# Optimization experiments

Measured on AMD Instinct MI355X. Metric: run time of the kernel, lower is better.

Reference implementation:

```python
import jax, jax.numpy as jnp
import numpy as np


def _lstm_layer(x, W_ih, W_hh, b_ih, b_hh):
    """Single unidirectional LSTM layer, PyTorch gate order (i, f, g, o).

    x: [B, T, I]; W_ih: [4H, I]; W_hh: [4H, H]; b_ih, b_hh: [4H].
    Returns all hidden states: [B, T, H].
    """
    B, T, _ = x.shape
    H = W_hh.shape[1]
    # Precompute input projections for all timesteps (one big GEMM): [B, T, 4H]
    x_proj = jnp.einsum('bti,gi->btg', x, W_ih) + b_ih + b_hh

    def step(carry, xt):
        h, c = carry
        gates = xt + h @ W_hh.T  # [B, 4H]
        i, f, g, o = jnp.split(gates, 4, axis=-1)
        c = jax.nn.sigmoid(f) * c + jax.nn.sigmoid(i) * jnp.tanh(g)
        h = jax.nn.sigmoid(o) * jnp.tanh(c)
        return (h, c), h

    init = (jnp.zeros((B, H), x.dtype), jnp.zeros((B, H), x.dtype))
    _, hs = jax.lax.scan(step, init, x_proj.transpose(1, 0, 2))  # hs: [T, B, H]
    return hs.transpose(1, 0, 2)


def setup_inputs() -> dict:
    key = jax.random.key(0)
    ks = jax.random.split(key, 16)
    B, C, T, F = 32, 4, 1024, 128
    I = C * F  # 512 = input_size
    H = 512   # hidden_size
    O = 80    # output_size (mel bins)
    s = 1.0 / np.sqrt(H)  # PyTorch LSTM/Linear init range
    inp = {'X_batch': jax.random.normal(ks[0], (B, C, T, F), jnp.float32)}
    in_sizes = [I, H, H]
    for l in range(3):
        k = 1 + 4 * l
        inp[f'W_ih_{l}'] = jax.random.uniform(ks[k + 0], (4 * H, in_sizes[l]), jnp.float32, -s, s)
        inp[f'W_hh_{l}'] = jax.random.uniform(ks[k + 1], (4 * H, H), jnp.float32, -s, s)
        inp[f'b_ih_{l}'] = jax.random.uniform(ks[k + 2], (4 * H,), jnp.float32, -s, s)
        inp[f'b_hh_{l}'] = jax.random.uniform(ks[k + 3], (4 * H,), jnp.float32, -s, s)
    inp['W_out'] = jax.random.uniform(ks[13], (O, H), jnp.float32, -s, s)
    inp['b_out'] = jax.random.uniform(ks[14], (O,), jnp.float32, -s, s)
    return inp


def reference(X_batch, W_ih_0, W_hh_0, b_ih_0, b_hh_0,
              W_ih_1, W_hh_1, b_ih_1, b_hh_1,
              W_ih_2, W_hh_2, b_ih_2, b_hh_2,
              W_out, b_out):
    B, C, T, F = X_batch.shape
    # [B, C, T, F] -> [B, T, C, F] -> [B, T, C*F], matching the torch permute+reshape
    x = X_batch.transpose(0, 2, 1, 3).reshape(B, T, C * F)
    layers = [(W_ih_0, W_hh_0, b_ih_0, b_hh_0),
              (W_ih_1, W_hh_1, b_ih_1, b_hh_1),
              (W_ih_2, W_hh_2, b_ih_2, b_hh_2)]
    for W_ih, W_hh, b_ih, b_hh in layers:
        x = _lstm_layer(x, W_ih, W_hh, b_ih, b_hh)
    last = x[:, -1, :]  # return_sequence=False: last timestep only, [B, H]
    # dropout is identity in eval mode
    return last @ W_out.T + b_out  # [B, O]
```

## Files before the change

### kernel.cpp

```cpp
#include <hip/hip_runtime.h>
#include <cstdint>


typedef unsigned short u16;
typedef _Float16 f16;
typedef f16 f16x8 __attribute__((ext_vector_type(8)));
typedef unsigned short ushort8 __attribute__((ext_vector_type(8)));
typedef float f32x4 __attribute__((ext_vector_type(4)));

#define NB 32
#define NT 1024
#define NH 512
#define N4H 2048
#define RR 16
#define MROWS (NB * NT)
#define HBUFB 8192

__device__ __forceinline__ float sigm(float x) { return 1.f / (1.f + __expf(-x)); }
__device__ __forceinline__ float tanh_s(float x) {
  float a = fabsf(x);
  float e = __expf(-2.f * a);
  float t = (1.f - e) / (1.f + e);
  return copysignf(t, x);
}

__device__ __forceinline__ void ld16_sc(const u16* p, uint4& d) {
  asm volatile("global_load_dwordx4 %0, %1, off sc0 sc1" : "=v"(d) : "v"(p));
}
__device__ __forceinline__ int ldf(const int* p) {
  int r;
  asm volatile("global_load_dword %0, %1, off sc0 sc1\n\ts_waitcnt vmcnt(0)"
               : "=v"(r) : "v"(p) : "memory");
  return r;
}
__device__ __forceinline__ void st16b_sc(u16* p, unsigned v) {
  asm volatile("global_store_short %0, %1, off sc0 sc1" :: "v"(p), "v"(v) : "memory");
}
__device__ __forceinline__ void st32b_sc(int* p, int v) {
  asm volatile("global_store_dword %0, %1, off sc0 sc1" :: "v"(p), "v"(v) : "memory");
}

__global__ void k_gather_x(const float* __restrict__ X, u16* __restrict__ xs) {
  int64_t i = (int64_t)blockIdx.x * 256 + threadIdx.x;
  int k = (int)(i & 511);
  int t = (int)((i >> 9) & 1023);
  int b = (int)(i >> 19);
  int c = k >> 7, f = k & 127;
  float v = X[(((int64_t)(b * 4 + c) * 1024 + t) << 7) + f];
  f16 hv = (f16)v;
  xs[((int64_t)b * 1024 + t) * 512 + k] = *(u16*)&hv;
}

__global__ void k_split_w(const float* __restrict__ W, u16* __restrict__ Wp) {
  int i = blockIdx.x * 256 + threadIdx.x;
  f16 hv = (f16)W[i];
  Wp[i] = *(u16*)&hv;
}

__global__ void k_bias(const float* __restrict__ bi, const float* __restrict__ bh,
                       float* __restrict__ bo) {
  int i = blockIdx.x * 256 + threadIdx.x;
  if (i < N4H) bo[i] = bi[i] + bh[i];
}

__launch_bounds__(256, 1)
__global__ void k_lstm3(const float* __restrict__ Whh0, const float* __restrict__ Whh1,
                        const float* __restrict__ Whh2,
                        const u16* __restrict__ Wp0, const u16* __restrict__ Wp1,
                        const u16* __restrict__ Wp2,
                        const float* __restrict__ bias0, const float* __restrict__ bias1,
                        const float* __restrict__ bias2,
                        const u16* __restrict__ xs, u16* __restrict__ hring,
                        u16* __restrict__ hfinal, int* __restrict__ flags) {
  __shared__ u16 wlds[32768];
  __shared__ u16 hbuf[16384];
  const int tid = threadIdx.x;
  const int lane = tid & 63;
  const int w = tid >> 6;
  const int wg = blockIdx.x;
  const int l = wg >> 6;
  const int wgl = wg & 63;
  const int bg = wgl >> 5;
  const int ugg = wgl & 31;
  const int q = lane >> 4;
  const int cb = lane & 15;
  const int tr = lane & 15;

  const float* Whh = (l == 0) ? Whh0 : (l == 1) ? Whh1 : Whh2;
  const u16* Wp = (l == 0) ? Wp0 : (l == 1) ? Wp1 : Wp2;
  const float* bs = (l == 0) ? bias0 : (l == 1) ? bias1 : bias2;

  const int64_t grow = (int64_t)(tr & 3) * 512 + ugg * 16 + w * 4 + (tr >> 2);

  f16x8 whh[16];
  {
    const float* wsrc = Whh + grow * 512 + q * 8;
#pragma unroll
    for (int kk = 0; kk < 16; ++kk) {
      float4 a = *(const float4*)(wsrc + kk * 32);
      float4 b = *(const float4*)(wsrc + kk * 32 + 4);
      f16x8 hv;
      hv[0] = (f16)a.x; hv[1] = (f16)a.y; hv[2] = (f16)a.z; hv[3] = (f16)a.w;
      hv[4] = (f16)b.x; hv[5] = (f16)b.y; hv[6] = (f16)b.z; hv[7] = (f16)b.w;
      whh[kk] = hv;
    }
  }

  {
#pragma unroll
    for (int i = 0; i < 16; ++i) {
      int c = tid + i * 256;
      int r = c >> 6;
      int kc = (c & 63) * 8;
      int tr2 = r & 15;
      int64_t gr = (int64_t)(tr2 & 3) * 512 + ugg * 16 + (r >> 4) * 4 + (tr2 >> 2);
      ushort8 v = *(const ushort8*)(Wp + gr * 512 + kc);
      *(ushort8*)&wlds[r * 512 + (kc ^ ((tr2 & 7) << 3))] = v;
    }
  }
  __syncthreads();

  const int bat = bg * 16 + cb;
  const int ucol = ugg * 16 + w * 4 + q;
  const float b0 = bs[ucol], b1 = bs[512 + ucol], b2 = bs[1024 + ucol],
              b3 = bs[1536 + ucol];
  float cst = 0.f;

  int* fl_own = flags + l * 64 + bg * 32;
  int* fl_up = flags + (l - 1) * 64 + bg * 32;
  int* fl_dn = flags + (l + 1) * 64 + bg * 32;
  const int wrow = (w * 16 + tr) * 512;
  const int wswz = (tr & 7) << 3;
  const int hswz = (cb & 7) << 3;
  const int hrbA = cb * 512;
  const int hrbB = HBUFB + cb * 512;

  for (int ts = 0; ts < NT; ++ts) {
    {
      const bool chk_own = (ts > 0);
      const bool chk_up = (l > 0);
      const bool chk_dn = (l < 2) && ((ts & 7) == 0);
      if (chk_own | chk_up | chk_dn) {
        int gd = 0;
        for (;;) {
          int ok = 1;
          if (chk_own) ok &= (ldf(fl_own + (lane & 31)) >= ts);
          if (chk_up) ok &= (ldf(fl_up + (lane & 31)) >= ts + 1);
          if (chk_dn) ok &= (ldf(fl_dn + (lane & 31)) >= ts - 8);
          if (__all(ok)) break;
          __builtin_amdgcn_s_sleep(2);
          if (++gd > (1 << 13)) break;
        }
      }
    }

    uint4 v[8];
    if (ts > 0) {
      const u16* srcA = hring + ((int64_t)(l * RR + ((ts - 1) & (RR - 1))) * NB
                                 + bg * 16) * 512;
#pragma unroll
      for (int i = 0; i < 4; ++i) {
        int c = tid + i * 256;
        int sb = c >> 6, so = (c & 63) * 8;
        ld16_sc(srcA + sb * 512 + so, v[i]);
      }
    }
    if (l == 0) {
      const u16* srcB = xs + ((int64_t)(bg * 16) * NT + ts) * 512;
#pragma unroll
      for (int i = 0; i < 4; ++i) {
        int c = tid + i * 256;
        int sb = c >> 6, so = (c & 63) * 8;
        ld16_sc(srcB + (int64_t)sb * NT * 512 + so, v[4 + i]);
      }
    } else {
      const u16* srcB = hring + ((int64_t)((l - 1) * RR + (ts & (RR - 1))) * NB
                                 + bg * 16) * 512;
#pragma unroll
      for (int i = 0; i < 4; ++i) {
        int c = tid + i * 256;
        int sb = c >> 6, so = (c & 63) * 8;
        ld16_sc(srcB + sb * 512 + so, v[4 + i]);
      }
    }
    asm volatile("s_waitcnt vmcnt(0)" ::: "memory");
    __builtin_amdgcn_sched_barrier(0);

    if (ts > 0) {
#pragma unroll
      for (int i = 0; i < 4; ++i) {
        int c = tid + i * 256;
        int sb = c >> 6, so = (c & 63) * 8;
        *(uint4*)&hbuf[sb * 512 + (so ^ ((sb & 7) << 3))] = v[i];
      }
    }
#pragma unroll
    for (int i = 0; i < 4; ++i) {
      int c = tid + i * 256;
      int sb = c >> 6, so = (c & 63) * 8;
      *(uint4*)&hbuf[HBUFB + sb * 512 + (so ^ ((sb & 7) << 3))] = v[4 + i];
    }
    __syncthreads();

    f32x4 acc = {0.f, 0.f, 0.f, 0.f};

    if (ts > 0) {
#pragma unroll
      for (int kk = 0; kk < 16; ++kk) {
        const int kidx = (kk * 32 + q * 8) ^ hswz;
        f16x8 hv = *(const f16x8*)&hbuf[hrbA + kidx];
        acc = __builtin_amdgcn_mfma_f32_16x16x32_f16(whh[kk], hv, acc, 0, 0, 0);
      }
    }

#pragma unroll
    for (int kk = 0; kk < 16; ++kk) {
      const int kv = kk * 32 + q * 8;
      f16x8 wv = *(const f16x8*)&wlds[wrow + (kv ^ wswz)];
      f16x8 xv = *(const f16x8*)&hbuf[hrbB + (kv ^ hswz)];
      acc = __builtin_amdgcn_mfma_f32_16x16x32_f16(wv, xv, acc, 0, 0, 0);
    }

    float ip = acc[0] + b0;
    float fp = acc[1] + b1;
    float gg = acc[2] + b2;
    float op = acc[3] + b3;
    float i_s = sigm(ip), f_s = sigm(fp), g_t = tanh_s(gg), o_s = sigm(op);
    cst = f_s * cst + i_s * g_t;
    float h = o_s * tanh_s(cst);

    f16 hf = (f16)h;
    u16 hbits = *(u16*)&hf;
    u16* hw = hring + ((int64_t)(l * RR + (ts & (RR - 1))) * NB + bat) * 512 + ucol;
    st16b_sc(hw, (unsigned)hbits);
    if (l == 2 && ts == NT - 1) hfinal[bat * 512 + ucol] = hbits;
    asm volatile("s_waitcnt vmcnt(0)" ::: "memory");
    __syncthreads();
    if (tid == 0) st32b_sc(flags + l * 64 + bg * 32 + ugg, ts + 1);
  }
}

__global__ void k_final(const u16* __restrict__ hfinal, const float* __restrict__ Wout,
                        const float* __restrict__ bout, float* __restrict__ out) {
  const int b = blockIdx.x;
  const int o = threadIdx.x;
  if (o >= 80) return;
  const u16* hp = hfinal + b * 512;
  float acc = bout[o];
  for (int k = 0; k < 512; ++k) {
    f16 hv = *(const f16*)&hp[k];
    acc += (float)hv * Wout[o * 512 + k];
  }
  out[b * 80 + o] = acc;
}

extern "C" void kernel_launch(void* const* d_in, const int* in_sizes, int n_in,
                              void* d_out, int out_size, void* d_ws, size_t ws_size,
                              hipStream_t stream) {
  const float* X = (const float*)d_in[0];
  const float* Wih[3] = {(const float*)d_in[1], (const float*)d_in[5], (const float*)d_in[9]};
  const float* Whh[3] = {(const float*)d_in[2], (const float*)d_in[6], (const float*)d_in[10]};
  const float* bih[3] = {(const float*)d_in[3], (const float*)d_in[7], (const float*)d_in[11]};
  const float* bhh[3] = {(const float*)d_in[4], (const float*)d_in[8], (const float*)d_in[12]};
  const float* Wout = (const float*)d_in[13];
  const float* bout = (const float*)d_in[14];
  float* out = (float*)d_out;

  char* ws = (char*)d_ws;
  size_t off = 0;
  auto alloc = [&](size_t bytes) {
    char* p = ws + off;
    off = (off + bytes + 255) & ~(size_t)255;
    return p;
  };
  u16* xs = (u16*)alloc((size_t)MROWS * 512 * 2);
  u16* Wp[3];
  for (int l = 0; l < 3; ++l) Wp[l] = (u16*)alloc((size_t)N4H * 512 * 2);
  float* bias[3];
  for (int l = 0; l < 3; ++l) bias[l] = (float*)alloc(N4H * 4);
  u16* hring = (u16*)alloc((size_t)3 * RR * NB * 512 * 2);
  u16* hfinal = (u16*)alloc(NB * 512 * 2);
  int* flags = (int*)alloc(3 * 64 * 4);

  hipMemsetAsync(flags, 0, 3 * 64 * 4, stream);
  k_gather_x<<<65536, 256, 0, stream>>>(X, xs);
  for (int l = 0; l < 3; ++l) {
    k_split_w<<<4096, 256, 0, stream>>>(Wih[l], Wp[l]);
    k_bias<<<8, 256, 0, stream>>>(bih[l], bhh[l], bias[l]);
  }

  k_lstm3<<<192, 256, 0, stream>>>(Whh[0], Whh[1], Whh[2],
                                   Wp[0], Wp[1], Wp[2],
                                   bias[0], bias[1], bias[2],
                                   xs, hring, hfinal, flags);

  k_final<<<32, 128, 0, stream>>>(hfinal, Wout, bout, out);
}
```

Before: 3.873 ms.

## Repartition LSTM workgroups to 8-batch groups with 32 units each

```diff
diff --git a/kernel.cpp b/kernel.cpp
--- a/kernel.cpp
+++ b/kernel.cpp
@@ -14,7 +14,7 @@
 #define N4H 2048
 #define RR 16
 #define MROWS (NB * NT)
-#define HBUFB 8192
+#define HBUFB 4096
 
 __device__ __forceinline__ float sigm(float x) { return 1.f / (1.f + __expf(-x)); }
 __device__ __forceinline__ float tanh_s(float x) {
@@ -72,28 +72,29 @@
                         const float* __restrict__ bias2,
                         const u16* __restrict__ xs, u16* __restrict__ hring,
                         u16* __restrict__ hfinal, int* __restrict__ flags) {
-  __shared__ u16 wlds[32768];
-  __shared__ u16 hbuf[16384];
+  __shared__ u16 wlds[65536];
+  __shared__ u16 hbuf[8192];
   const int tid = threadIdx.x;
   const int lane = tid & 63;
   const int w = tid >> 6;
   const int wg = blockIdx.x;
   const int l = wg >> 6;
   const int wgl = wg & 63;
-  const int bg = wgl >> 5;
-  const int ugg = wgl & 31;
+  const int bg = wgl >> 4;
+  const int ugg = wgl & 15;
   const int q = lane >> 4;
   const int cb = lane & 15;
   const int tr = lane & 15;
+  const int cbm = cb & 7;
 
   const float* Whh = (l == 0) ? Whh0 : (l == 1) ? Whh1 : Whh2;
   const u16* Wp = (l == 0) ? Wp0 : (l == 1) ? Wp1 : Wp2;
   const float* bs = (l == 0) ? bias0 : (l == 1) ? bias1 : bias2;
 
-  const int64_t grow = (int64_t)(tr & 3) * 512 + ugg * 16 + w * 4 + (tr >> 2);
-
-  f16x8 whh[16];
-  {
+  f16x8 whh[2][16];
+#pragma unroll
+  for (int t = 0; t < 2; ++t) {
+    const int64_t grow = (int64_t)(tr & 3) * 512 + ugg * 32 + w * 8 + t * 4 + (tr >> 2);
     const float* wsrc = Whh + grow * 512 + q * 8;
 #pragma unroll
     for (int kk = 0; kk < 16; ++kk) {
@@ -102,51 +103,82 @@
       f16x8 hv;
       hv[0] = (f16)a.x; hv[1] = (f16)a.y; hv[2] = (f16)a.z; hv[3] = (f16)a.w;
       hv[4] = (f16)b.x; hv[5] = (f16)b.y; hv[6] = (f16)b.z; hv[7] = (f16)b.w;
-      whh[kk] = hv;
+      whh[t][kk] = hv;
     }
   }
 
   {
 #pragma unroll
-    for (int i = 0; i < 16; ++i) {
+    for (int i = 0; i < 32; ++i) {
       int c = tid + i * 256;
       int r = c >> 6;
       int kc = (c & 63) * 8;
-      int tr2 = r & 15;
-      int64_t gr = (int64_t)(tr2 & 3) * 512 + ugg * 16 + (r >> 4) * 4 + (tr2 >> 2);
+      int w2 = r >> 5, t2 = (r >> 4) & 1, tr2 = r & 15;
+      int64_t gr = (int64_t)(tr2 & 3) * 512 + ugg * 32 + w2 * 8 + t2 * 4 + (tr2 >> 2);
       ushort8 v = *(const ushort8*)(Wp + gr * 512 + kc);
       *(ushort8*)&wlds[r * 512 + (kc ^ ((tr2 & 7) << 3))] = v;
     }
   }
   __syncthreads();
 
-  const int bat = bg * 16 + cb;
-  const int ucol = ugg * 16 + w * 4 + q;
-  const float b0 = bs[ucol], b1 = bs[512 + ucol], b2 = bs[1024 + ucol],
-              b3 = bs[1536 + ucol];
-  float cst = 0.f;
-
-  int* fl_own = flags + l * 64 + bg * 32;
-  int* fl_up = flags + (l - 1) * 64 + bg * 32;
-  int* fl_dn = flags + (l + 1) * 64 + bg * 32;
-  const int wrow = (w * 16 + tr) * 512;
-  const int wswz = (tr & 7) << 3;
-  const int hswz = (cb & 7) << 3;
-  const int hrbA = cb * 512;
-  const int hrbB = HBUFB + cb * 512;
+  const int bat = bg * 8 + cbm;
+  const bool owner = (cb < 8);
+  int ucol[2];
+  float bv[2][4];
+#pragma unroll
+  for (int t = 0; t < 2; ++t) {
+    ucol[t] = ugg * 32 + w * 8 + t * 4 + q;
+#pragma unroll
+    for (int j = 0; j < 4; ++j) bv[t][j] = bs[j * 512 + ucol[t]];
+  }
+  float cst0 = 0.f, cst1 = 0.f;
+
+  int* fl_own = flags + l * 64 + bg * 16;
+  int* fl_up = flags + (l - 1) * 64 + bg * 16;
+  int* fl_dn = flags + (l + 1) * 64 + bg * 16;
+  const int hswz = cbm << 3;
+  const int hrbA = cbm * 512;
+  const int hrbB = HBUFB + cbm * 512;
 
   for (int ts = 0; ts < NT; ++ts) {
+    if (l > 0) {
+      int gd = 0;
+      for (;;) {
+        if (__all((int)(ldf(fl_up + (lane & 15)) >= ts + 1))) break;
+        __builtin_amdgcn_s_sleep(2);
+        if (++gd > (1 << 13)) break;
+      }
+    }
+
+    uint4 v[4];
+    if (l == 0) {
+      const u16* srcB = xs + ((int64_t)(bg * 8) * NT + ts) * 512;
+#pragma unroll
+      for (int i = 0; i < 2; ++i) {
+        int c = tid + i * 256;
+        int sb = c >> 6, so = (c & 63) * 8;
+        ld16_sc(srcB + (int64_t)sb * NT * 512 + so, v[2 + i]);
+      }
+    } else {
+      const u16* srcB = hring + ((int64_t)((l - 1) * RR + (ts & (RR - 1))) * NB
+                                 + bg * 8) * 512;
+#pragma unroll
+      for (int i = 0; i < 2; ++i) {
+        int c = tid + i * 256;
+        int sb = c >> 6, so = (c & 63) * 8;
+        ld16_sc(srcB + sb * 512 + so, v[2 + i]);
+      }
+    }
+
     {
       const bool chk_own = (ts > 0);
-      const bool chk_up = (l > 0);
       const bool chk_dn = (l < 2) && ((ts & 7) == 0);
-      if (chk_own | chk_up | chk_dn) {
+      if (chk_own | chk_dn) {
         int gd = 0;
         for (;;) {
           int ok = 1;
-          if (chk_own) ok &= (ldf(fl_own + (lane & 31)) >= ts);
-          if (chk_up) ok &= (ldf(fl_up + (lane & 31)) >= ts + 1);
-          if (chk_dn) ok &= (ldf(fl_dn + (lane & 31)) >= ts - 8);
+          if (chk_own) ok &= (ldf(fl_own + (lane & 15)) >= ts);
+          if (chk_dn) ok &= (ldf(fl_dn + (lane & 15)) >= ts - 8);
           if (__all(ok)) break;
           __builtin_amdgcn_s_sleep(2);
           if (++gd > (1 << 13)) break;
@@ -154,89 +186,88 @@
       }
     }
 
-    uint4 v[8];
     if (ts > 0) {
       const u16* srcA = hring + ((int64_t)(l * RR + ((ts - 1) & (RR - 1))) * NB
-                                 + bg * 16) * 512;
-#pragma unroll
-      for (int i = 0; i < 4; ++i) {
+                                 + bg * 8) * 512;
+#pragma unroll
+      for (int i = 0; i < 2; ++i) {
         int c = tid + i * 256;
         int sb = c >> 6, so = (c & 63) * 8;
         ld16_sc(srcA + sb * 512 + so, v[i]);
       }
     }
-    if (l == 0) {
-      const u16* srcB = xs + ((int64_t)(bg * 16) * NT + ts) * 512;
-#pragma unroll
-      for (int i = 0; i < 4; ++i) {
-        int c = tid + i * 256;
-        int sb = c >> 6, so = (c & 63) * 8;
-        ld16_sc(srcB + (int64_t)sb * NT * 512 + so, v[4 + i]);
-      }
-    } else {
-      const u16* srcB = hring + ((int64_t)((l - 1) * RR + (ts & (RR - 1))) * NB
-                                 + bg * 16) * 512;
-#pragma unroll
-      for (int i = 0; i < 4; ++i) {
-        int c = tid + i * 256;
-        int sb = c >> 6, so = (c & 63) * 8;
-        ld16_sc(srcB + sb * 512 + so, v[4 + i]);
-      }
-    }
     asm volatile("s_waitcnt vmcnt(0)" ::: "memory");
     __builtin_amdgcn_sched_barrier(0);
 
     if (ts > 0) {
 #pragma unroll
-      for (int i = 0; i < 4; ++i) {
+      for (int i = 0; i < 2; ++i) {
         int c = tid + i * 256;
         int sb = c >> 6, so = (c & 63) * 8;
         *(uint4*)&hbuf[sb * 512 + (so ^ ((sb & 7) << 3))] = v[i];
       }
     }
 #pragma unroll
-    for (int i = 0; i < 4; ++i) {
+    for (int i = 0; i < 2; ++i) {
       int c = tid + i * 256;
       int sb = c >> 6, so = (c & 63) * 8;
-      *(uint4*)&hbuf[HBUFB + sb * 512 + (so ^ ((sb & 7) << 3))] = v[4 + i];
+      *(uint4*)&hbuf[HBUFB + sb * 512 + (so ^ ((sb & 7) << 3))] = v[2 + i];
     }
     __syncthreads();
 
-    f32x4 acc = {0.f, 0.f, 0.f, 0.f};
+    f32x4 acc0 = {0.f, 0.f, 0.f, 0.f};
+    f32x4 acc1 = {0.f, 0.f, 0.f, 0.f};
 
     if (ts > 0) {
 #pragma unroll
       for (int kk = 0; kk < 16; ++kk) {
         const int kidx = (kk * 32 + q * 8) ^ hswz;
         f16x8 hv = *(const f16x8*)&hbuf[hrbA + kidx];
-        acc = __builtin_amdgcn_mfma_f32_16x16x32_f16(whh[kk], hv, acc, 0, 0, 0);
+        acc0 = __builtin_amdgcn_mfma_f32_16x16x32_f16(whh[0][kk], hv, acc0, 0, 0, 0);
+        acc1 = __builtin_amdgcn_mfma_f32_16x16x32_f16(whh[1][kk], hv, acc1, 0, 0, 0);
       }
     }
 
 #pragma unroll
     for (int kk = 0; kk < 16; ++kk) {
       const int kv = kk * 32 + q * 8;
-      f16x8 wv = *(const f16x8*)&wlds[wrow + (kv ^ wswz)];
       f16x8 xv = *(const f16x8*)&hbuf[hrbB + (kv ^ hswz)];
-      acc = __builtin_amdgcn_mfma_f32_16x16x32_f16(wv, xv, acc, 0, 0, 0);
-    }
-
-    float ip = acc[0] + b0;
-    float fp = acc[1] + b1;
-    float gg = acc[2] + b2;
-    float op = acc[3] + b3;
-    float i_s = sigm(ip), f_s = sigm(fp), g_t = tanh_s(gg), o_s = sigm(op);
-    cst = f_s * cst + i_s * g_t;
-    float h = o_s * tanh_s(cst);
-
-    f16 hf = (f16)h;
-    u16 hbits = *(u16*)&hf;
-    u16* hw = hring + ((int64_t)(l * RR + (ts & (RR - 1))) * NB + bat) * 512 + ucol;
-    st16b_sc(hw, (unsigned)hbits);
-    if (l == 2 && ts == NT - 1) hfinal[bat * 512 + ucol] = hbits;
+      f16x8 wv0 = *(const f16x8*)&wlds[(w * 32 + tr) * 512 + (kv ^ ((tr & 7) << 3))];
+      f16x8 wv1 = *(const f16x8*)&wlds[(w * 32 + 16 + tr) * 512 + (kv ^ ((tr & 7) << 3))];
+      acc0 = __builtin_amdgcn_mfma_f32_16x16x32_f16(wv0, xv, acc0, 0, 0, 0);
+      acc1 = __builtin_amdgcn_mfma_f32_16x16x32_f16(wv1, xv, acc1, 0, 0, 0);
+    }
+
+    u16 hb0, hb1;
+    {
+      float ip = acc0[0] + bv[0][0], fp = acc0[1] + bv[0][1];
+      float gg = acc0[2] + bv[0][2], op = acc0[3] + bv[0][3];
+      float i_s = sigm(ip), f_s = sigm(fp), g_t = tanh_s(gg), o_s = sigm(op);
+      cst0 = f_s * cst0 + i_s * g_t;
+      f16 hf = (f16)(o_s * tanh_s(cst0));
+      hb0 = *(u16*)&hf;
+    }
+    {
+      float ip = acc1[0] + bv[1][0], fp = acc1[1] + bv[1][1];
+      float gg = acc1[2] + bv[1][2], op = acc1[3] + bv[1][3];
+      float i_s = sigm(ip), f_s = sigm(fp), g_t = tanh_s(gg), o_s = sigm(op);
+      cst1 = f_s * cst1 + i_s * g_t;
+      f16 hf = (f16)(o_s * tanh_s(cst1));
+      hb1 = *(u16*)&hf;
+    }
+
+    if (owner) {
+      u16* hw = hring + ((int64_t)(l * RR + (ts & (RR - 1))) * NB + bat) * 512;
+      st16b_sc(hw + ucol[0], (unsigned)hb0);
+      st16b_sc(hw + ucol[1], (unsigned)hb1);
+      if (l == 2 && ts == NT - 1) {
+        hfinal[bat * 512 + ucol[0]] = hb0;
+        hfinal[bat * 512 + ucol[1]] = hb1;
+      }
+    }
     asm volatile("s_waitcnt vmcnt(0)" ::: "memory");
     __syncthreads();
-    if (tid == 0) st32b_sc(flags + l * 64 + bg * 32 + ugg, ts + 1);
+    if (tid == 0) st32b_sc(flags + l * 64 + bg * 16 + ugg, ts + 1);
   }
 }
 
```

After: 4.812 ms. +24.3%, slower.

## Prefetch next-step input and compute input projection before recurrent wait

Applied to the files above, without the earlier changes.

```diff
diff --git a/kernel.cpp b/kernel.cpp
--- a/kernel.cpp
+++ b/kernel.cpp
@@ -135,90 +135,82 @@
   const int hrbA = cb * 512;
   const int hrbB = HBUFB + cb * 512;
 
+  int sbv[4], sov[4];
+#pragma unroll
+  for (int i = 0; i < 4; ++i) {
+    int c = tid + i * 256;
+    sbv[i] = c >> 6;
+    sov[i] = (c & 63) * 8;
+  }
+
+  uint4 vB[4], vA[4];
+  if (l > 0) {
+    int gd = 0;
+    for (;;) {
+      if (__all((int)(ldf(fl_up + (lane & 31)) >= 1))) break;
+      __builtin_amdgcn_s_sleep(1);
+      if (++gd > (1 << 14)) break;
+    }
+    const u16* srcB = hring + ((int64_t)((l - 1) * RR) * NB + bg * 16) * 512;
+#pragma unroll
+    for (int i = 0; i < 4; ++i) ld16_sc(srcB + sbv[i] * 512 + sov[i], vB[i]);
+  } else {
+    const u16* srcB = xs + ((int64_t)(bg * 16) * NT) * 512;
+#pragma unroll
+    for (int i = 0; i < 4; ++i)
+      ld16_sc(srcB + (int64_t)sbv[i] * NT * 512 + sov[i], vB[i]);
+  }
+
   for (int ts = 0; ts < NT; ++ts) {
+    asm volatile("s_waitcnt vmcnt(0)" ::: "memory");
+    __builtin_amdgcn_sched_barrier(0);
+#pragma unroll
+    for (int i = 0; i < 4; ++i)
+      *(uint4*)&hbuf[HBUFB + sbv[i] * 512 + (sov[i] ^ ((sbv[i] & 7) << 3))] = vB[i];
+    __syncthreads();
+
+    f32x4 acc = {0.f, 0.f, 0.f, 0.f};
+#pragma unroll
+    for (int kk = 0; kk < 16; ++kk) {
+      const int kv = kk * 32 + q * 8;
+      f16x8 wv = *(const f16x8*)&wlds[wrow + (kv ^ wswz)];
+      f16x8 xv = *(const f16x8*)&hbuf[hrbB + (kv ^ hswz)];
+      acc = __builtin_amdgcn_mfma_f32_16x16x32_f16(wv, xv, acc, 0, 0, 0);
+    }
+
     {
       const bool chk_own = (ts > 0);
-      const bool chk_up = (l > 0);
       const bool chk_dn = (l < 2) && ((ts & 7) == 0);
-      if (chk_own | chk_up | chk_dn) {
+      if (chk_own | chk_dn) {
         int gd = 0;
         for (;;) {
           int ok = 1;
           if (chk_own) ok &= (ldf(fl_own + (lane & 31)) >= ts);
-          if (chk_up) ok &= (ldf(fl_up + (lane & 31)) >= ts + 1);
           if (chk_dn) ok &= (ldf(fl_dn + (lane & 31)) >= ts - 8);
           if (__all(ok)) break;
-          __builtin_amdgcn_s_sleep(2);
-          if (++gd > (1 << 13)) break;
+          __builtin_amdgcn_s_sleep(1);
+          if (++gd > (1 << 14)) break;
         }
       }
     }
 
-    uint4 v[8];
     if (ts > 0) {
       const u16* srcA = hring + ((int64_t)(l * RR + ((ts - 1) & (RR - 1))) * NB
                                  + bg * 16) * 512;
 #pragma unroll
-      for (int i = 0; i < 4; ++i) {
-        int c = tid + i * 256;
-        int sb = c >> 6, so = (c & 63) * 8;
-        ld16_sc(srcA + sb * 512 + so, v[i]);
-      }
-    }
-    if (l == 0) {
-      const u16* srcB = xs + ((int64_t)(bg * 16) * NT + ts) * 512;
-#pragma unroll
-      for (int i = 0; i < 4; ++i) {
-        int c = tid + i * 256;
-        int sb = c >> 6, so = (c & 63) * 8;
-        ld16_sc(srcB + (int64_t)sb * NT * 512 + so, v[4 + i]);
-      }
-    } else {
-      const u16* srcB = hring + ((int64_t)((l - 1) * RR + (ts & (RR - 1))) * NB
-                                 + bg * 16) * 512;
-#pragma unroll
-      for (int i = 0; i < 4; ++i) {
-        int c = tid + i * 256;
-        int sb = c >> 6, so = (c & 63) * 8;
-        ld16_sc(srcB + sb * 512 + so, v[4 + i]);
-      }
-    }
-    asm volatile("s_waitcnt vmcnt(0)" ::: "memory");
-    __builtin_amdgcn_sched_barrier(0);
-
-    if (ts > 0) {
-#pragma unroll
-      for (int i = 0; i < 4; ++i) {
-        int c = tid + i * 256;
-        int sb = c >> 6, so = (c & 63) * 8;
-        *(uint4*)&hbuf[sb * 512 + (so ^ ((sb & 7) << 3))] = v[i];
-      }
-    }
-#pragma unroll
-    for (int i = 0; i < 4; ++i) {
-      int c = tid + i * 256;
-      int sb = c >> 6, so = (c & 63) * 8;
-      *(uint4*)&hbuf[HBUFB + sb * 512 + (so ^ ((sb & 7) << 3))] = v[4 + i];
-    }
-    __syncthreads();
-
-    f32x4 acc = {0.f, 0.f, 0.f, 0.f};
-
-    if (ts > 0) {
+      for (int i = 0; i < 4; ++i) ld16_sc(srcA + sbv[i] * 512 + sov[i], vA[i]);
+      asm volatile("s_waitcnt vmcnt(0)" ::: "memory");
+      __builtin_amdgcn_sched_barrier(0);
+#pragma unroll
+      for (int i = 0; i < 4; ++i)
+        *(uint4*)&hbuf[sbv[i] * 512 + (sov[i] ^ ((sbv[i] & 7) << 3))] = vA[i];
+      __syncthreads();
 #pragma unroll
       for (int kk = 0; kk < 16; ++kk) {
         const int kidx = (kk * 32 + q * 8) ^ hswz;
         f16x8 hv = *(const f16x8*)&hbuf[hrbA + kidx];
         acc = __builtin_amdgcn_mfma_f32_16x16x32_f16(whh[kk], hv, acc, 0, 0, 0);
       }
-    }
-
-#pragma unroll
-    for (int kk = 0; kk < 16; ++kk) {
-      const int kv = kk * 32 + q * 8;
-      f16x8 wv = *(const f16x8*)&wlds[wrow + (kv ^ wswz)];
-      f16x8 xv = *(const f16x8*)&hbuf[hrbB + (kv ^ hswz)];
-      acc = __builtin_amdgcn_mfma_f32_16x16x32_f16(wv, xv, acc, 0, 0, 0);
     }
 
     float ip = acc[0] + b0;
@@ -237,6 +229,26 @@
     asm volatile("s_waitcnt vmcnt(0)" ::: "memory");
     __syncthreads();
     if (tid == 0) st32b_sc(flags + l * 64 + bg * 32 + ugg, ts + 1);
+
+    if (ts + 1 < NT) {
+      if (l > 0) {
+        int gd = 0;
+        for (;;) {
+          if (__all((int)(ldf(fl_up + (lane & 31)) >= ts + 2))) break;
+          __builtin_amdgcn_s_sleep(1);
+          if (++gd > (1 << 14)) break;
+        }
+        const u16* srcB = hring + ((int64_t)((l - 1) * RR + ((ts + 1) & (RR - 1))) * NB
+                                   + bg * 16) * 512;
+#pragma unroll
+        for (int i = 0; i < 4; ++i) ld16_sc(srcB + sbv[i] * 512 + sov[i], vB[i]);
+      } else {
+        const u16* srcB = xs + ((int64_t)(bg * 16) * NT + (ts + 1)) * 512;
+#pragma unroll
+        for (int i = 0; i < 4; ++i)
+          ld16_sc(srcB + (int64_t)sbv[i] * NT * 512 + sov[i], vB[i]);
+      }
+    }
   }
 }
 
```

New measurement: 3.266 ms. -15.7%, faster.
